# Kernel optimization log

Hardware: AMD Instinct MI355X
Metric: run time of the kernel (lower is better)

The kernel has to match this reference:

```python
import jax, jax.numpy as jnp
import numpy as np

N_NODES = 200000
F = 256
B = 8192
FAN1 = 16  # hop-1 fanout (layer_num_samples[0])
FAN2 = 4   # hop-2 fanout (layer_num_samples[1])


def setup_inputs() -> dict:
    key = jax.random.key(0)
    k1, k2, k3, k4, k5, k6 = jax.random.split(key, 6)
    node_feats = jax.random.normal(k1, (N_NODES, F), dtype=jnp.float32)
    # SageLayer weight: [out_size, 2*layer_size]
    W1 = jax.random.normal(k2, (F, 2 * F), dtype=jnp.float32) * 0.05
    W2 = jax.random.normal(k3, (F, 2 * F), dtype=jnp.float32) * 0.05
    batch_nodes = jax.random.randint(k4, (B,), 0, N_NODES)
    neigh1 = jax.random.randint(k5, (B, FAN1), 0, N_NODES)
    M1 = B + B * FAN1  # layer-1 node set: batch nodes + their sampled neighbors
    neigh2 = jax.random.randint(k6, (M1, FAN2), 0, N_NODES)
    return {"node_feats": node_feats, "W1": W1, "W2": W2,
            "batch_nodes": batch_nodes, "neigh1": neigh1, "neigh2": neigh2}


def reference(node_feats, W1, W2, batch_nodes, neigh1, neigh2):
    b = batch_nodes.shape[0]
    # layer-1 node list: batch nodes first, then hop-1 neighbors (row-major)
    nodes1 = jnp.concatenate([batch_nodes, neigh1.reshape(-1)])  # [17B]
    # ---- SAGE layer 1: MEAN-aggregate hop-2 neighbor raw features ----
    agg1 = node_feats[neigh2].mean(axis=1)              # [17B, F]
    self1 = node_feats[nodes1]                           # [17B, F]
    h1 = jax.nn.relu(jnp.concatenate([self1, agg1], axis=1) @ W1.T)  # [17B, F]
    # ---- SAGE layer 2: MEAN-aggregate hop-1 neighbors' hidden embs ----
    agg2 = h1[b:].reshape(b, neigh1.shape[1], -1).mean(axis=1)  # [B, F]
    h_self = h1[:b]                                      # [B, F]
    out = jax.nn.relu(jnp.concatenate([h_self, agg2], axis=1) @ W2.T)  # [B, F]
    return out
```

## Files before the change

### kernel.cpp

```cpp
#include <hip/hip_runtime.h>
#include <hip/hip_bf16.h>

#define NB 8192
#define M1T 139264

typedef __attribute__((ext_vector_type(8))) short bf16x8;
typedef __attribute__((ext_vector_type(16))) float f32x16;

__device__ __forceinline__ unsigned short f2b(float f) {
  union { float f; unsigned u; } v; v.f = f;
  unsigned r = v.u + 0x7fffu + ((v.u >> 16) & 1u);
  return (unsigned short)(r >> 16);
}
__device__ __forceinline__ float b2f(unsigned u16) {
  union { unsigned u; float f; } v; v.u = u16 << 16;
  return v.f;
}
__device__ __forceinline__ uint4 pack8u(float a0, float a1, float a2, float a3,
                                        float a4, float a5, float a6, float a7) {
  uint4 v;
  v.x = (unsigned)f2b(a0) | ((unsigned)f2b(a1) << 16);
  v.y = (unsigned)f2b(a2) | ((unsigned)f2b(a3) << 16);
  v.z = (unsigned)f2b(a4) | ((unsigned)f2b(a5) << 16);
  v.w = (unsigned)f2b(a6) | ((unsigned)f2b(a7) << 16);
  return v;
}

#define GLDS16(g, l)                                                          \
  __builtin_amdgcn_global_load_lds(                                           \
      (const __attribute__((address_space(1))) unsigned int*)(const void*)(g),\
      (__attribute__((address_space(3))) unsigned int*)(void*)(l), 16, 0, 0)

__global__ void convert_w(const float* __restrict__ W1, const float* __restrict__ W2,
                          unsigned short* __restrict__ W1s, unsigned short* __restrict__ W2s) {
  int i = blockIdx.x * 256 + threadIdx.x;
  const float* W; unsigned short* out; int f4;
  if (i < 32768) { W = W1; out = W1s; f4 = i; }
  else           { W = W2; out = W2s; f4 = i - 32768; }
  int n  = (f4 * 4) >> 9;
  int c0 = (f4 * 4) & 511;
  int kt = c0 >> 6;
  int slot = (c0 & 63) >> 3;
  int e  = c0 & 7;
  int sw = slot ^ (n & 7);
  float4 v = *((const float4*)W + f4);
  ushort4 o;
  o.x = f2b(v.x); o.y = f2b(v.y); o.z = f2b(v.z); o.w = f2b(v.w);
  *(ushort4*)(out + kt * 16384 + n * 64 + sw * 8 + e) = o;
}

__global__ __launch_bounds__(512, 4)
void sage_l1(const float* __restrict__ feats,
             const unsigned short* __restrict__ Wbs,
             const int* __restrict__ batch_nodes,
             const int* __restrict__ neigh1,
             const int* __restrict__ neigh2,
             unsigned short* __restrict__ h1b)
{
  __shared__ __align__(16) unsigned short As[2][64 * 64];
  __shared__ __align__(16) unsigned short Bs[2][256 * 64];
  const int tid = threadIdx.x;
  const int m0 = blockIdx.x * 64;
  const int w = tid >> 6, lane = tid & 63, l31 = lane & 31, lh = lane >> 5;
  const int mh = w & 1, nq = w >> 1;
  const int m = tid >> 3, slot = tid & 7;
  const int r = m0 + m;

  const int self = (r < NB) ? batch_nodes[r] : neigh1[r - NB];
  const int4 nb = *(const int4*)(neigh2 + (size_t)r * 4);
  const char* fb = (const char*)feats;
  const unsigned so  = (unsigned)self * 1024u + (unsigned)slot * 32u;
  const unsigned no0 = (unsigned)nb.x * 1024u + (unsigned)slot * 32u;
  const unsigned no1 = (unsigned)nb.y * 1024u + (unsigned)slot * 32u;
  const unsigned no2 = (unsigned)nb.z * 1024u + (unsigned)slot * 32u;
  const unsigned no3 = (unsigned)nb.w * 1024u + (unsigned)slot * 32u;
  const int arowC = mh * 32 + l31;
  const int n0C = nq * 64 + l31, n1C = n0C + 32;

  f32x16 acc0 = {}, acc1 = {};
  float4 a0[8], a1[8];

  #define L1_LOADS(KT, AR)                                                    \
    do { if ((KT) < 4) {                                                      \
           AR[0] = *(const float4*)(fb + so + (KT) * 256);                    \
           AR[1] = *(const float4*)(fb + so + (KT) * 256 + 16);               \
         } else {                                                             \
           const int _kb = ((KT) - 4) * 256;                                  \
           AR[0] = *(const float4*)(fb + no0 + _kb);                          \
           AR[1] = *(const float4*)(fb + no0 + _kb + 16);                     \
           AR[2] = *(const float4*)(fb + no1 + _kb);                          \
           AR[3] = *(const float4*)(fb + no1 + _kb + 16);                     \
           AR[4] = *(const float4*)(fb + no2 + _kb);                          \
           AR[5] = *(const float4*)(fb + no2 + _kb + 16);                     \
           AR[6] = *(const float4*)(fb + no3 + _kb);                          \
           AR[7] = *(const float4*)(fb + no3 + _kb + 16);                     \
         } } while (0)

  #define L1_BISSUE(KT)                                                       \
    do { const unsigned short* _s = Wbs + (size_t)(KT) * 16384;               \
         unsigned short* _d = &Bs[(KT) & 1][0];                               \
         _Pragma("unroll")                                                    \
         for (int _q = 0; _q < 4; ++_q) {                                     \
           int _i = _q * 512 + tid;                                           \
           GLDS16(_s + (size_t)_i * 8, _d + _i * 8);                          \
         } } while (0)

  #define L1_CONV(KT, AR, AV)                                                 \
    do { if ((KT) < 4) {                                                      \
           AV = pack8u(AR[0].x, AR[0].y, AR[0].z, AR[0].w,                    \
                       AR[1].x, AR[1].y, AR[1].z, AR[1].w);                   \
         } else {                                                             \
           float s0 = AR[0].x + AR[2].x + AR[4].x + AR[6].x;                  \
           float s1 = AR[0].y + AR[2].y + AR[4].y + AR[6].y;                  \
           float s2 = AR[0].z + AR[2].z + AR[4].z + AR[6].z;                  \
           float s3 = AR[0].w + AR[2].w + AR[4].w + AR[6].w;                  \
           float s4 = AR[1].x + AR[3].x + AR[5].x + AR[7].x;                  \
           float s5 = AR[1].y + AR[3].y + AR[5].y + AR[7].y;                  \
           float s6 = AR[1].z + AR[3].z + AR[5].z + AR[7].z;                  \
           float s7 = AR[1].w + AR[3].w + AR[5].w + AR[7].w;                  \
           AV = pack8u(s0 * 0.25f, s1 * 0.25f, s2 * 0.25f, s3 * 0.25f,       \
                       s4 * 0.25f, s5 * 0.25f, s6 * 0.25f, s7 * 0.25f);      \
         } } while (0)

  #define L1_STEP(KT, AR, NCNT)                                               \
    do { uint4 _av;                                                           \
         L1_CONV(KT, AR, _av);      \
         *(uint4*)(&As[(KT) & 1][m * 64 + ((slot ^ (m & 7)) << 3)]) = _av;    \
         asm volatile("s_waitcnt vmcnt(" #NCNT ") lgkmcnt(0)" ::: "memory");  \
         __builtin_amdgcn_s_barrier();                                        \
         if ((KT) < 7) L1_BISSUE((KT) + 1);                                   \
         if ((KT) < 6) L1_LOADS((KT) + 2, AR);                                \
         __builtin_amdgcn_sched_barrier(0);                                   \
         __builtin_amdgcn_s_setprio(1);                                       \
         _Pragma("unroll")                                                    \
         for (int _kk = 0; _kk < 4; ++_kk) {                                  \
           int _sl = _kk * 2 + lh;                                            \
           bf16x8 _a  = *(const bf16x8*)(&As[(KT) & 1][arowC * 64 + ((_sl ^ (arowC & 7)) << 3)]); \
           bf16x8 _b0 = *(const bf16x8*)(&Bs[(KT) & 1][n0C * 64 + ((_sl ^ (n0C & 7)) << 3)]);     \
           bf16x8 _b1 = *(const bf16x8*)(&Bs[(KT) & 1][n1C * 64 + ((_sl ^ (n1C & 7)) << 3)]);     \
           acc0 = __builtin_amdgcn_mfma_f32_32x32x16_bf16(_a, _b0, acc0, 0, 0, 0);                \
           acc1 = __builtin_amdgcn_mfma_f32_32x32x16_bf16(_a, _b1, acc1, 0, 0, 0);                \
         }                                                                    \
         __builtin_amdgcn_s_setprio(0);                                       \
    } while (0)

  L1_LOADS(0, a0);
  L1_BISSUE(0);
  L1_LOADS(1, a1);
  __builtin_amdgcn_sched_barrier(0);

  L1_STEP(0, a0, 2);
  L1_STEP(1, a1, 2);
  L1_STEP(2, a0, 2);
  L1_STEP(3, a1, 8);
  L1_STEP(4, a0, 8);
  L1_STEP(5, a1, 8);
  L1_STEP(6, a0, 8);
  L1_STEP(7, a1, 0);

  #undef L1_LOADS
  #undef L1_BISSUE
  #undef L1_CONV
  #undef L1_STEP

  #pragma unroll
  for (int q = 0; q < 16; ++q) {
    int row = m0 + mh * 32 + (q & 3) + 8 * (q >> 2) + 4 * lh;
    int col0 = nq * 64 + l31;
    float v0 = acc0[q], v1 = acc1[q];
    v0 = v0 > 0.f ? v0 : 0.f;
    v1 = v1 > 0.f ? v1 : 0.f;
    h1b[(size_t)row * 256 + col0] = f2b(v0);
    h1b[(size_t)row * 256 + col0 + 32] = f2b(v1);
  }
}

__global__ __launch_bounds__(512, 4)
void sage_l2(const unsigned short* __restrict__ h1b,
             const unsigned short* __restrict__ Wbs,
             float* __restrict__ out)
{
  __shared__ __align__(16) unsigned short As[2][32 * 64];
  __shared__ __align__(16) unsigned short Bs[2][256 * 64];
  const int tid = threadIdx.x;
  const int m0 = blockIdx.x * 32;
  const int w = tid >> 6, lane = tid & 63, l31 = lane & 31, lh = lane >> 5;
  const int m = tid >> 4, slot = tid & 15;
  const int r = m0 + m;
  const char* hb = (const char*)h1b;
  const unsigned so = (unsigned)r * 512u + (unsigned)slot * 8u;
  const unsigned ao = (unsigned)(NB + r * 16) * 512u + (unsigned)slot * 8u;
  const int arowC = l31;
  const int n0C = w * 32 + l31;

  f32x16 acc = {};
  uint2 b0r[16], b1r[16];

  #define L2_LOADS(KT, BR)                                                    \
    do { if ((KT) < 4) {                                                      \
           BR[0] = *(const uint2*)(hb + so + (KT) * 128);                     \
         } else {                                                             \
           _Pragma("unroll")                                                  \
           for (int _j = 0; _j < 16; ++_j)                                    \
             BR[_j] = *(const uint2*)(hb + ao + _j * 512 + ((KT) - 4) * 128); \
         } } while (0)

  #define L2_BISSUE(KT)                                                       \
    do { const unsigned short* _s = Wbs + (size_t)(KT) * 16384;               \
         unsigned short* _d = &Bs[(KT) & 1][0];                               \
         _Pragma("unroll")                                                    \
         for (int _q = 0; _q < 4; ++_q) {                                     \
           int _i = _q * 512 + tid;                                           \
           GLDS16(_s + (size_t)_i * 8, _d + _i * 8);                          \
         } } while (0)

  #define L2_CONV(KT, BR, AV)                                                 \
    do { if ((KT) < 4) { AV = BR[0]; }                                        \
         else {                                                               \
           float s0 = 0, s1 = 0, s2 = 0, s3 = 0;                              \
           _Pragma("unroll")                                                  \
           for (int _j = 0; _j < 16; ++_j) {                                  \
             s0 += b2f(BR[_j].x & 0xffffu); s1 += b2f(BR[_j].x >> 16);        \
             s2 += b2f(BR[_j].y & 0xffffu); s3 += b2f(BR[_j].y >> 16);        \
           }                                                                  \
           const float _q16 = 1.0f / 16.0f;                                   \
           AV.x = (unsigned)f2b(s0 * _q16) | ((unsigned)f2b(s1 * _q16) << 16);\
           AV.y = (unsigned)f2b(s2 * _q16) | ((unsigned)f2b(s3 * _q16) << 16);\
         } } while (0)

  #define L2_STEP(KT, BR, NCNT)                                               \
    do { uint2 _av;                                                           \
         L2_CONV(KT, BR, _av);                                                \
         *(uint2*)(&As[(KT) & 1][m * 64 + (((slot >> 1) ^ (m & 7)) << 3) + (slot & 1) * 4]) = _av; \
         asm volatile("s_waitcnt vmcnt(" #NCNT ") lgkmcnt(0)" ::: "memory");  \
         __builtin_amdgcn_s_barrier();                                        \
         if ((KT) < 7) L2_BISSUE((KT) + 1);                                   \
         if ((KT) < 6) L2_LOADS((KT) + 2, BR);                                \
         __builtin_amdgcn_sched_barrier(0);                                   \
         __builtin_amdgcn_s_setprio(1);                                       \
         _Pragma("unroll")                                                    \
         for (int _kk = 0; _kk < 4; ++_kk) {                                  \
           int _sl = _kk * 2 + lh;                                            \
           bf16x8 _a = *(const bf16x8*)(&As[(KT) & 1][arowC * 64 + ((_sl ^ (arowC & 7)) << 3)]); \
           bf16x8 _b = *(const bf16x8*)(&Bs[(KT) & 1][n0C * 64 + ((_sl ^ (n0C & 7)) << 3)]);     \
           acc = __builtin_amdgcn_mfma_f32_32x32x16_bf16(_a, _b, acc, 0, 0, 0);                  \
         }                                                                    \
         __builtin_amdgcn_s_setprio(0);                                       \
    } while (0)

  L2_LOADS(0, b0r);
  L2_BISSUE(0);
  L2_LOADS(1, b1r);
  __builtin_amdgcn_sched_barrier(0);

  L2_STEP(0, b0r, 1);
  L2_STEP(1, b1r, 1);
  L2_STEP(2, b0r, 1);
  L2_STEP(3, b1r, 16);
  L2_STEP(4, b0r, 16);
  L2_STEP(5, b1r, 16);
  L2_STEP(6, b0r, 16);
  L2_STEP(7, b1r, 0);

  #undef L2_LOADS
  #undef L2_BISSUE
  #undef L2_CONV
  #undef L2_STEP

  #pragma unroll
  for (int q = 0; q < 16; ++q) {
    int row = m0 + (q & 3) + 8 * (q >> 2) + 4 * lh;
    int col = n0C;
    float v = acc[q];
    out[(size_t)row * 256 + col] = v > 0.f ? v : 0.f;
  }
}

extern "C" void kernel_launch(void* const* d_in, const int* in_sizes, int n_in,
                              void* d_out, int out_size, void* d_ws, size_t ws_size,
                              hipStream_t stream) {
  const float* feats       = (const float*)d_in[0];
  const float* W1          = (const float*)d_in[1];
  const float* W2          = (const float*)d_in[2];
  const int*   batch_nodes = (const int*)d_in[3];
  const int*   neigh1      = (const int*)d_in[4];
  const int*   neigh2      = (const int*)d_in[5];
  float* out = (float*)d_out;

  unsigned short* W1s = (unsigned short*)d_ws;
  unsigned short* W2s = W1s + 131072;
  unsigned short* h1b = W2s + 131072;

  hipLaunchKernelGGL(convert_w, dim3(256), dim3(256), 0, stream, W1, W2, W1s, W2s);
  hipLaunchKernelGGL(sage_l1, dim3(M1T / 64), dim3(512), 0, stream,
                     feats, W1s, batch_nodes, neigh1, neigh2, h1b);
  hipLaunchKernelGGL(sage_l2, dim3(NB / 32), dim3(512), 0, stream, h1b, W2s, out);
}
```

Baseline: 153.9 us.

## Fuse layer-2 mean aggregation into layer-1 epilogue and simplify layer-2 GEMM

The layer-1 kernel now writes a compact [B,512] activation matrix for layer 2. Self blocks store the relu'd hidden rows into the first half. Neighbour blocks reduce each group of 16 rows to its mean in registers, using a cross-half shuffle, and store it into the second half. This avoids writing and re-reading the full 17B×256 h1 tensor and removes the gather-and-average from layer 2. Layer 2 becomes a plain GEMM that loads A tiles straight into LDS, with 256 threads and two accumulators per wave, at the cost of a simpler single-stage pipeline that syncs on every step.

```diff
diff --git a/kernel.cpp b/kernel.cpp
--- a/kernel.cpp
+++ b/kernel.cpp
@@ -3,6 +3,7 @@
 
 #define NB 8192
 #define M1T 139264
+#define SELFB 128
 
 typedef __attribute__((ext_vector_type(8))) short bf16x8;
 typedef __attribute__((ext_vector_type(16))) float f32x16;
@@ -11,10 +12,6 @@
   union { float f; unsigned u; } v; v.f = f;
   unsigned r = v.u + 0x7fffu + ((v.u >> 16) & 1u);
   return (unsigned short)(r >> 16);
-}
-__device__ __forceinline__ float b2f(unsigned u16) {
-  union { unsigned u; float f; } v; v.u = u16 << 16;
-  return v.f;
 }
 __device__ __forceinline__ uint4 pack8u(float a0, float a1, float a2, float a3,
                                         float a4, float a5, float a6, float a7) {
@@ -55,7 +52,7 @@
              const int* __restrict__ batch_nodes,
              const int* __restrict__ neigh1,
              const int* __restrict__ neigh2,
-             unsigned short* __restrict__ h1b)
+             unsigned short* __restrict__ A2)
 {
   __shared__ __align__(16) unsigned short As[2][64 * 64];
   __shared__ __align__(16) unsigned short Bs[2][256 * 64];
@@ -163,20 +160,42 @@
   #undef L1_CONV
   #undef L1_STEP
 
-  #pragma unroll
-  for (int q = 0; q < 16; ++q) {
-    int row = m0 + mh * 32 + (q & 3) + 8 * (q >> 2) + 4 * lh;
-    int col0 = nq * 64 + l31;
-    float v0 = acc0[q], v1 = acc1[q];
-    v0 = v0 > 0.f ? v0 : 0.f;
-    v1 = v1 > 0.f ? v1 : 0.f;
-    h1b[(size_t)row * 256 + col0] = f2b(v0);
-    h1b[(size_t)row * 256 + col0 + 32] = f2b(v1);
+  if (blockIdx.x < SELFB) {
+    #pragma unroll
+    for (int q = 0; q < 16; ++q) {
+      int row = m0 + mh * 32 + (q & 3) + 8 * (q >> 2) + 4 * lh;
+      int col0 = nq * 64 + l31;
+      float v0 = acc0[q], v1 = acc1[q];
+      v0 = v0 > 0.f ? v0 : 0.f;
+      v1 = v1 > 0.f ? v1 : 0.f;
+      A2[(size_t)row * 512 + col0] = f2b(v0);
+      A2[(size_t)row * 512 + col0 + 32] = f2b(v1);
+    }
+  } else {
+    const int bi = blockIdx.x - SELFB;
+    #pragma unroll
+    for (int gi = 0; gi < 2; ++gi) {
+      float sA = 0.f, sB = 0.f;
+      #pragma unroll
+      for (int q = gi * 8; q < gi * 8 + 8; ++q) {
+        float v0 = acc0[q], v1 = acc1[q];
+        sA += (v0 > 0.f ? v0 : 0.f);
+        sB += (v1 > 0.f ? v1 : 0.f);
+      }
+      sA += __shfl_xor(sA, 32, 64);
+      sB += __shfl_xor(sB, 32, 64);
+      if (lh == 0) {
+        int gr = bi * 4 + mh * 2 + gi;
+        int col = 256 + nq * 64 + l31;
+        A2[(size_t)gr * 512 + col] = f2b(sA * 0.0625f);
+        A2[(size_t)gr * 512 + col + 32] = f2b(sB * 0.0625f);
+      }
+    }
   }
 }
 
-__global__ __launch_bounds__(512, 4)
-void sage_l2(const unsigned short* __restrict__ h1b,
+__global__ __launch_bounds__(256, 2)
+void sage_l2(const unsigned short* __restrict__ A2,
              const unsigned short* __restrict__ Wbs,
              float* __restrict__ out)
 {
@@ -185,94 +204,53 @@
   const int tid = threadIdx.x;
   const int m0 = blockIdx.x * 32;
   const int w = tid >> 6, lane = tid & 63, l31 = lane & 31, lh = lane >> 5;
-  const int m = tid >> 4, slot = tid & 15;
-  const int r = m0 + m;
-  const char* hb = (const char*)h1b;
-  const unsigned so = (unsigned)r * 512u + (unsigned)slot * 8u;
-  const unsigned ao = (unsigned)(NB + r * 16) * 512u + (unsigned)slot * 8u;
+  const int mA = tid >> 3, swA = tid & 7;
   const int arowC = l31;
-  const int n0C = w * 32 + l31;
-
-  f32x16 acc = {};
-  uint2 b0r[16], b1r[16];
-
-  #define L2_LOADS(KT, BR)                                                    \
-    do { if ((KT) < 4) {                                                      \
-           BR[0] = *(const uint2*)(hb + so + (KT) * 128);                     \
-         } else {                                                             \
-           _Pragma("unroll")                                                  \
-           for (int _j = 0; _j < 16; ++_j)                                    \
-             BR[_j] = *(const uint2*)(hb + ao + _j * 512 + ((KT) - 4) * 128); \
-         } } while (0)
-
-  #define L2_BISSUE(KT)                                                       \
+  const int n0C = w * 64 + l31, n1C = n0C + 32;
+  const unsigned short* aSrc = A2 + (size_t)(m0 + mA) * 512 + (swA ^ (mA & 7)) * 8;
+
+  f32x16 acc0 = {}, acc1 = {};
+
+  #define L2_STAGE(KT)                                                        \
     do { const unsigned short* _s = Wbs + (size_t)(KT) * 16384;               \
          unsigned short* _d = &Bs[(KT) & 1][0];                               \
          _Pragma("unroll")                                                    \
-         for (int _q = 0; _q < 4; ++_q) {                                     \
-           int _i = _q * 512 + tid;                                           \
+         for (int _q = 0; _q < 8; ++_q) {                                     \
+           int _i = _q * 256 + tid;                                           \
            GLDS16(_s + (size_t)_i * 8, _d + _i * 8);                          \
-         } } while (0)
-
-  #define L2_CONV(KT, BR, AV)                                                 \
-    do { if ((KT) < 4) { AV = BR[0]; }                                        \
-         else {                                                               \
-           float s0 = 0, s1 = 0, s2 = 0, s3 = 0;                              \
-           _Pragma("unroll")                                                  \
-           for (int _j = 0; _j < 16; ++_j) {                                  \
-             s0 += b2f(BR[_j].x & 0xffffu); s1 += b2f(BR[_j].x >> 16);        \
-             s2 += b2f(BR[_j].y & 0xffffu); s3 += b2f(BR[_j].y >> 16);        \
-           }                                                                  \
-           const float _q16 = 1.0f / 16.0f;                                   \
-           AV.x = (unsigned)f2b(s0 * _q16) | ((unsigned)f2b(s1 * _q16) << 16);\
-           AV.y = (unsigned)f2b(s2 * _q16) | ((unsigned)f2b(s3 * _q16) << 16);\
-         } } while (0)
-
-  #define L2_STEP(KT, BR, NCNT)                                               \
-    do { uint2 _av;                                                           \
-         L2_CONV(KT, BR, _av);                                                \
-         *(uint2*)(&As[(KT) & 1][m * 64 + (((slot >> 1) ^ (m & 7)) << 3) + (slot & 1) * 4]) = _av; \
-         asm volatile("s_waitcnt vmcnt(" #NCNT ") lgkmcnt(0)" ::: "memory");  \
-         __builtin_amdgcn_s_barrier();                                        \
-         if ((KT) < 7) L2_BISSUE((KT) + 1);                                   \
-         if ((KT) < 6) L2_LOADS((KT) + 2, BR);                                \
-         __builtin_amdgcn_sched_barrier(0);                                   \
-         __builtin_amdgcn_s_setprio(1);                                       \
-         _Pragma("unroll")                                                    \
-         for (int _kk = 0; _kk < 4; ++_kk) {                                  \
-           int _sl = _kk * 2 + lh;                                            \
-           bf16x8 _a = *(const bf16x8*)(&As[(KT) & 1][arowC * 64 + ((_sl ^ (arowC & 7)) << 3)]); \
-           bf16x8 _b = *(const bf16x8*)(&Bs[(KT) & 1][n0C * 64 + ((_sl ^ (n0C & 7)) << 3)]);     \
-           acc = __builtin_amdgcn_mfma_f32_32x32x16_bf16(_a, _b, acc, 0, 0, 0);                  \
          }                                                                    \
-         __builtin_amdgcn_s_setprio(0);                                       \
+         GLDS16(aSrc + (KT) * 64, &As[(KT) & 1][mA * 64 + swA * 8]);          \
     } while (0)
 
-  L2_LOADS(0, b0r);
-  L2_BISSUE(0);
-  L2_LOADS(1, b1r);
-  __builtin_amdgcn_sched_barrier(0);
-
-  L2_STEP(0, b0r, 1);
-  L2_STEP(1, b1r, 1);
-  L2_STEP(2, b0r, 1);
-  L2_STEP(3, b1r, 16);
-  L2_STEP(4, b0r, 16);
-  L2_STEP(5, b1r, 16);
-  L2_STEP(6, b0r, 16);
-  L2_STEP(7, b1r, 0);
-
-  #undef L2_LOADS
-  #undef L2_BISSUE
-  #undef L2_CONV
-  #undef L2_STEP
+  L2_STAGE(0);
+  asm volatile("s_waitcnt vmcnt(0)" ::: "memory");
+  __builtin_amdgcn_s_barrier();
+
+  #pragma unroll
+  for (int kt = 0; kt < 8; ++kt) {
+    if (kt < 7) L2_STAGE(kt + 1);
+    __builtin_amdgcn_s_setprio(1);
+    #pragma unroll
+    for (int kk = 0; kk < 4; ++kk) {
+      int sl = kk * 2 + lh;
+      bf16x8 a  = *(const bf16x8*)(&As[kt & 1][arowC * 64 + ((sl ^ (arowC & 7)) << 3)]);
+      bf16x8 b0 = *(const bf16x8*)(&Bs[kt & 1][n0C * 64 + ((sl ^ (n0C & 7)) << 3)]);
+      bf16x8 b1 = *(const bf16x8*)(&Bs[kt & 1][n1C * 64 + ((sl ^ (n1C & 7)) << 3)]);
+      acc0 = __builtin_amdgcn_mfma_f32_32x32x16_bf16(a, b0, acc0, 0, 0, 0);
+      acc1 = __builtin_amdgcn_mfma_f32_32x32x16_bf16(a, b1, acc1, 0, 0, 0);
+    }
+    __builtin_amdgcn_s_setprio(0);
+    asm volatile("s_waitcnt vmcnt(0)" ::: "memory");
+    __builtin_amdgcn_s_barrier();
+  }
+  #undef L2_STAGE
 
   #pragma unroll
   for (int q = 0; q < 16; ++q) {
     int row = m0 + (q & 3) + 8 * (q >> 2) + 4 * lh;
-    int col = n0C;
-    float v = acc[q];
-    out[(size_t)row * 256 + col] = v > 0.f ? v : 0.f;
+    float v0 = acc0[q], v1 = acc1[q];
+    out[(size_t)row * 256 + n0C] = v0 > 0.f ? v0 : 0.f;
+    out[(size_t)row * 256 + n1C] = v1 > 0.f ? v1 : 0.f;
   }
 }
 
@@ -289,10 +267,10 @@
 
   unsigned short* W1s = (unsigned short*)d_ws;
   unsigned short* W2s = W1s + 131072;
-  unsigned short* h1b = W2s + 131072;
+  unsigned short* A2  = W2s + 131072;
 
   hipLaunchKernelGGL(convert_w, dim3(256), dim3(256), 0, stream, W1, W2, W1s, W2s);
   hipLaunchKernelGGL(sage_l1, dim3(M1T / 64), dim3(512), 0, stream,
-                     feats, W1s, batch_nodes, neigh1, neigh2, h1b);
-  hipLaunchKernelGGL(sage_l2, dim3(NB / 32), dim3(512), 0, stream, h1b, W2s, out);
-}
+                     feats, W1s, batch_nodes, neigh1, neigh2, A2);
+  hipLaunchKernelGGL(sage_l2, dim3(NB / 32), dim3(256), 0, stream, A2, W2s, out);
+}
```

New measurement: 126.9 us, median of 2. 1.21x faster.
